# Performance work log

Hardware: AMD Instinct MI355X
Metric: run time of the kernel (lower is better)

## Reference

```python
import jax, jax.numpy as jnp
import numpy as np

REP_DIM = 256
ATT_DIM = 256
AGRU_DIM = 256
BATCH = 64
MAX_FACTS = 512


def setup_inputs() -> dict:
    key = jax.random.key(0)
    ks = jax.random.split(key, 16)

    def lin(k, out_d, in_d):
        return jax.random.normal(k, (out_d, in_d), dtype=jnp.float32) / np.sqrt(in_d)

    inp = {
        "queries": jax.random.normal(ks[0], (BATCH, 1, REP_DIM), dtype=jnp.float32),
        "facts": jax.random.normal(ks[1], (BATCH, MAX_FACTS, REP_DIM), dtype=jnp.float32),
        "num_facts": jax.random.randint(ks[2], (BATCH,), 1, MAX_FACTS + 1, dtype=jnp.int32),
        "m_old": jax.random.normal(ks[3], (BATCH, 1, REP_DIM), dtype=jnp.float32),
        # attention MLP
        "W1_w": lin(ks[4], ATT_DIM, 4 * REP_DIM),
        "W1_b": jnp.zeros((ATT_DIM,), jnp.float32),
        "W2_w": lin(ks[5], 1, ATT_DIM),
        "W2_b": jnp.zeros((1,), jnp.float32),
        # attention GRU cell
        "Wr_w": lin(ks[6], AGRU_DIM, REP_DIM),
        "Ur_w": lin(ks[7], AGRU_DIM, AGRU_DIM),
        "Ur_b": jnp.zeros((AGRU_DIM,), jnp.float32),
        "Wg_w": lin(ks[8], AGRU_DIM, REP_DIM),
        "Ug_w": lin(ks[9], AGRU_DIM, AGRU_DIM),
        "Ug_b": jnp.zeros((AGRU_DIM,), jnp.float32),
        # output transform
        "Wt_w": lin(ks[10], REP_DIM, 2 * REP_DIM + AGRU_DIM),
        "Wt_b": jnp.zeros((REP_DIM,), jnp.float32),
    }
    return inp


def _forward(queries, facts, num_facts, m_old,
             W1_w, W1_b, W2_w, W2_b,
             Wr_w, Ur_w, Ur_b, Wg_w, Ug_w, Ug_b,
             Wt_w, Wt_b):
    B, T, D = facts.shape

    # ---- attention scores ----
    q = queries  # (B,1,D) broadcasts
    m = m_old
    z = jnp.concatenate(
        [facts * q, facts * m, jnp.abs(facts - q), jnp.abs(facts - m)], axis=2
    )  # (B,T,4D)
    Z = jnp.tanh(jnp.einsum("btf,af->bta", z, W1_w) + W1_b)
    Z = jnp.einsum("bta,oa->bto", Z, W2_w) + W2_b  # (B,T,1)
    mask = (jnp.arange(T)[None, :] < num_facts[:, None])[..., None]  # (B,T,1)
    Z = jnp.where(mask, Z, -jnp.inf)
    g = jax.nn.softmax(Z, axis=1)  # (B,T,1)

    # ---- attention GRU (sequential scan over facts) ----
    h0 = m_old[:, 0]  # (B,A)

    def step(h, xs):
        fact, g_t = xs  # (B,D), (B,1)
        r = jax.nn.sigmoid(fact @ Wr_w.T + h @ Ur_w.T + Ur_b)
        h_t = jnp.tanh(fact @ Wg_w.T + r * (h @ Ug_w.T + Ug_b))
        h_new = g_t * h_t + (1.0 - g_t) * h
        return h_new, h_new

    xs = (jnp.swapaxes(facts, 0, 1), jnp.swapaxes(g, 0, 1))  # (T,B,D),(T,B,1)
    _, states = jax.lax.scan(step, h0, xs)  # (T,B,A)
    c = jnp.take_along_axis(
        states, (num_facts - 1)[None, :, None].astype(jnp.int32), axis=0
    )[0]  # (B,A)

    # ---- next memory ----
    cat = jnp.concatenate([m_old[:, 0], c, queries[:, 0]], axis=1)
    m_new = jax.nn.relu(cat @ Wt_w.T + Wt_b)
    return m_new[:, None, :]  # (B,1,D)


def reference(queries, facts, num_facts, m_old,
              W1_w, W1_b, W2_w, W2_b,
              Wr_w, Ur_w, Ur_b, Wg_w, Ug_w, Ug_b,
              Wt_w, Wt_b):
    return _forward(queries, facts, num_facts, m_old,
                    W1_w, W1_b, W2_w, W2_b,
                    Wr_w, Ur_w, Ur_b, Wg_w, Ug_w, Ug_b,
                    Wt_w, Wt_b)
```

## Files before the change

### kernel.cpp

```cpp
#include <hip/hip_runtime.h>
#include <hip/hip_fp16.h>
#include <stdint.h>

#define B 64
#define T 512
#define D 256

typedef _Float16 f16;
typedef __attribute__((ext_vector_type(8))) _Float16 f16x8;
typedef __attribute__((ext_vector_type(2))) _Float16 f16x2;
typedef __attribute__((ext_vector_type(4))) float f32x4;
typedef __attribute__((ext_vector_type(4))) unsigned int u32x4;

static __device__ __forceinline__ float dot2f(f16x2 a, f16x2 b, float c) {
  return __builtin_amdgcn_fdot2(a, b, c, false);
}
static __device__ __forceinline__ f16x2 as_h2(unsigned int u) {
  return __builtin_bit_cast(f16x2, u);
}

__global__ void k_convert(const float* __restrict__ W1, const float* __restrict__ Wr,
                          const float* __restrict__ Wg, const float* __restrict__ facts,
                          f16* __restrict__ W1h, f16* __restrict__ Wrh,
                          f16* __restrict__ Wgh, f16* __restrict__ Fh)
{
  const int64_t n1 = 256 * 1024, n2 = 65536, n3 = 65536, n4 = (int64_t)B * T * D;
  int64_t stride = (int64_t)gridDim.x * blockDim.x;
  for (int64_t i = (int64_t)blockIdx.x * blockDim.x + threadIdx.x; i < n1 + n2 + n3 + n4; i += stride) {
    if (i < n1)                W1h[i] = (f16)W1[i];
    else if (i < n1 + n2)      Wrh[i - n1] = (f16)Wr[i - n1];
    else if (i < n1 + n2 + n3) Wgh[i - n1 - n2] = (f16)Wg[i - n1 - n2];
    else                       Fh[i - n1 - n2 - n3] = (f16)facts[i - n1 - n2 - n3];
  }
}

__global__ __launch_bounds__(256, 2) void k_attn(
    const float* __restrict__ facts, const float* __restrict__ queries,
    const float* __restrict__ m_old, const f16* __restrict__ W1h,
    const float* __restrict__ W1_b, const float* __restrict__ W2_w,
    const float* __restrict__ W2_b, float* __restrict__ Zlog)
{
  const int b = blockIdx.y;
  const int t0 = blockIdx.x * 32;
  const int tid = threadIdx.x;
  const int lane = tid & 63;
  const int wave = tid >> 6;
  const int lr = lane & 15;
  const int lg = lane >> 4;

  __shared__ float q_s[D], m_s[D];
  __shared__ __align__(16) char zbuf[32 * 2048];
  __shared__ float part[4][32];

  q_s[tid] = queries[b * D + tid];
  m_s[tid] = m_old[b * D + tid];
  __syncthreads();

  for (int e = tid; e < 32 * 128; e += 256) {
    int t = e >> 7;
    int j2 = e & 127;
    int j = j2 * 2;
    const float2 f2 = *(const float2*)(facts + ((int64_t)(b * T) + t0 + t) * D + j);
    float q0 = q_s[j], q1 = q_s[j + 1], mm0 = m_s[j], mm1 = m_s[j + 1];
    f16x2 z0; z0[0] = (f16)(f2.x * q0);        z0[1] = (f16)(f2.y * q1);
    f16x2 z1; z1[0] = (f16)(f2.x * mm0);       z1[1] = (f16)(f2.y * mm1);
    f16x2 z2; z2[0] = (f16)fabsf(f2.x - q0);   z2[1] = (f16)fabsf(f2.y - q1);
    f16x2 z3; z3[0] = (f16)fabsf(f2.x - mm0);  z3[1] = (f16)fabsf(f2.y - mm1);
    int xr = (t & 7) << 4;
    int base = t * 2048;
    *(f16x2*)(zbuf + ((base + (0 * 128 + j2) * 4) ^ xr)) = z0;
    *(f16x2*)(zbuf + ((base + (1 * 128 + j2) * 4) ^ xr)) = z1;
    *(f16x2*)(zbuf + ((base + (2 * 128 + j2) * 4) ^ xr)) = z2;
    *(f16x2*)(zbuf + ((base + (3 * 128 + j2) * 4) ^ xr)) = z3;
  }
  __syncthreads();

  const int n0 = wave * 64;
  f32x4 acc[2][4];
  #pragma unroll
  for (int i = 0; i < 2; ++i)
    #pragma unroll
    for (int j = 0; j < 4; ++j) acc[i][j] = (f32x4){0.f, 0.f, 0.f, 0.f};

  #pragma unroll 2
  for (int ks = 0; ks < 32; ++ks) {
    f16x8 af[2];
    #pragma unroll
    for (int mt = 0; mt < 2; ++mt) {
      int row = mt * 16 + lr;
      int byte = (row * 2048 + ks * 64 + lg * 16) ^ ((row & 7) << 4);
      af[mt] = *(const f16x8*)(zbuf + byte);
    }
    #pragma unroll
    for (int nt = 0; nt < 4; ++nt) {
      int a = n0 + nt * 16 + lr;
      f16x8 bf = *(const f16x8*)(W1h + (int64_t)a * 1024 + ks * 32 + lg * 8);
      acc[0][nt] = __builtin_amdgcn_mfma_f32_16x16x32_f16(af[0], bf, acc[0][nt], 0, 0, 0);
      acc[1][nt] = __builtin_amdgcn_mfma_f32_16x16x32_f16(af[1], bf, acc[1][nt], 0, 0, 0);
    }
  }

  float pr[2][4] = {{0.f, 0.f, 0.f, 0.f}, {0.f, 0.f, 0.f, 0.f}};
  #pragma unroll
  for (int nt = 0; nt < 4; ++nt) {
    int a = n0 + nt * 16 + lr;
    float b1 = W1_b[a];
    float w2 = W2_w[a];
    #pragma unroll
    for (int mt = 0; mt < 2; ++mt)
      #pragma unroll
      for (int r = 0; r < 4; ++r)
        pr[mt][r] += tanhf(acc[mt][nt][r] + b1) * w2;
  }
  #pragma unroll
  for (int mt = 0; mt < 2; ++mt)
    #pragma unroll
    for (int r = 0; r < 4; ++r) {
      float v = pr[mt][r];
      v += __shfl_xor(v, 1, 64);
      v += __shfl_xor(v, 2, 64);
      v += __shfl_xor(v, 4, 64);
      v += __shfl_xor(v, 8, 64);
      pr[mt][r] = v;
    }
  if ((lane & 15) == 0) {
    #pragma unroll
    for (int mt = 0; mt < 2; ++mt)
      #pragma unroll
      for (int r = 0; r < 4; ++r)
        part[wave][mt * 16 + lg * 4 + r] = pr[mt][r];
  }
  __syncthreads();
  if (tid < 32)
    Zlog[b * T + t0 + tid] = part[0][tid] + part[1][tid] + part[2][tid] + part[3][tid] + W2_b[0];
}

__global__ __launch_bounds__(256, 2) void k_factproj(
    const f16* __restrict__ Fh, const f16* __restrict__ Wrh, const f16* __restrict__ Wgh,
    const float* __restrict__ Ur_b, float* __restrict__ Fr, float* __restrict__ Fg)
{
  const int b = blockIdx.y;
  const int t0 = blockIdx.x * 64;
  const int tid = threadIdx.x;
  const int lane = tid & 63;
  const int wave = tid >> 6;
  const int lr = lane & 15;
  const int lg = lane >> 4;

  __shared__ __align__(16) char albuf[64 * 512];

  for (int c = tid; c < 64 * 32; c += 256) {
    int row = c >> 5;
    int kc = c & 31;
    f16x8 v = *(const f16x8*)(Fh + ((int64_t)(b * T) + t0 + row) * D + kc * 8);
    int byte = (row * 512 + kc * 16) ^ ((row & 7) << 4);
    *(f16x8*)(albuf + byte) = v;
  }
  __syncthreads();

  f32x4 accr[16], accg[16];
  #pragma unroll
  for (int i = 0; i < 16; ++i) { accr[i] = (f32x4){0.f,0.f,0.f,0.f}; accg[i] = (f32x4){0.f,0.f,0.f,0.f}; }

  const int arow = wave * 16 + lr;
  #pragma unroll 2
  for (int ks = 0; ks < 8; ++ks) {
    int byte = (arow * 512 + ks * 64 + lg * 16) ^ ((arow & 7) << 4);
    f16x8 af = *(const f16x8*)(albuf + byte);
    #pragma unroll
    for (int nt = 0; nt < 16; ++nt) {
      int a = nt * 16 + lr;
      f16x8 br = *(const f16x8*)(Wrh + a * 256 + ks * 32 + lg * 8);
      f16x8 bg = *(const f16x8*)(Wgh + a * 256 + ks * 32 + lg * 8);
      accr[nt] = __builtin_amdgcn_mfma_f32_16x16x32_f16(af, br, accr[nt], 0, 0, 0);
      accg[nt] = __builtin_amdgcn_mfma_f32_16x16x32_f16(af, bg, accg[nt], 0, 0, 0);
    }
  }

  #pragma unroll
  for (int nt = 0; nt < 16; ++nt) {
    int col = nt * 16 + lr;
    float urb = Ur_b[col];
    #pragma unroll
    for (int r = 0; r < 4; ++r) {
      int t = t0 + wave * 16 + lg * 4 + r;
      int64_t off = ((int64_t)(b * T) + t) * D + col;
      Fr[off] = accr[nt][r] + urb;
      Fg[off] = accg[nt][r];
    }
  }
}

__global__ void k_softmax2(const float* __restrict__ Zlog, const int* __restrict__ num_facts,
                           float* __restrict__ g)
{
  const int b = blockIdx.x;
  const int lane = threadIdx.x;
  const int nf = num_facts[b];
  float v[8];
  float mx = -INFINITY;
  #pragma unroll
  for (int j = 0; j < 8; ++j) {
    int t = j * 64 + lane;
    float z = Zlog[b * T + t];
    v[j] = (t < nf) ? z : -INFINITY;
    mx = fmaxf(mx, v[j]);
  }
  #pragma unroll
  for (int s = 1; s < 64; s <<= 1) mx = fmaxf(mx, __shfl_xor(mx, s, 64));
  float e[8];
  float sum = 0.f;
  #pragma unroll
  for (int j = 0; j < 8; ++j) {
    int t = j * 64 + lane;
    e[j] = (t < nf) ? __expf(v[j] - mx) : 0.f;
    sum += e[j];
  }
  #pragma unroll
  for (int s = 1; s < 64; s <<= 1) sum += __shfl_xor(sum, s, 64);
  float inv = 1.f / sum;
  #pragma unroll
  for (int j = 0; j < 8; ++j)
    g[b * T + j * 64 + lane] = e[j] * inv;
}

__global__ __launch_bounds__(512, 2) void k_scan_v3(
    const float* __restrict__ Fr, const float* __restrict__ Fg, const float* __restrict__ g,
    const int* __restrict__ num_facts, const float* __restrict__ Ur_w,
    const float* __restrict__ Ug_w, const float* __restrict__ Ug_b,
    const float* __restrict__ m_old, float* __restrict__ c_out)
{
  const int b = blockIdx.x;
  const int tid = threadIdx.x;
  const int row = ((tid >> 6) << 5) + (tid & 31);
  const int kgh = (tid >> 5) & 1;
  const int nf = num_facts[b];

  __shared__ __align__(16) f16 hbuf[2][256];

  const float* __restrict__ urow = Ur_w + (int64_t)row * 256 + kgh * 128;
  const float* __restrict__ grow = Ug_w + (int64_t)row * 256 + kgh * 128;
  f16x2 wR[64], wG[64];
  #pragma unroll
  for (int j = 0; j < 64; ++j) {
    float2 a = *(const float2*)(urow + 2 * j);
    float2 c = *(const float2*)(grow + 2 * j);
    f16x2 pa; pa[0] = (f16)a.x; pa[1] = (f16)a.y; wR[j] = pa;
    f16x2 pc; pc[0] = (f16)c.x; pc[1] = (f16)c.y; wG[j] = pc;
  }
  const float ugb = Ug_b[row];
  float h = m_old[b * 256 + row];
  if (kgh == 0) hbuf[0][row] = (f16)h;
  __syncthreads();

  const float* __restrict__ FrP = Fr + (int64_t)(b * T) * D + row;
  const float* __restrict__ FgP = Fg + (int64_t)(b * T) * D + row;
  const float* __restrict__ gP  = g + b * T;
  float fr = FrP[0], fg = FgP[0], gt = gP[0];

  const f16* hc = hbuf[0];
  f16* hn = hbuf[1];

  for (int t = 0; t < nf; ++t) {
    float fr_n = 0.f, fg_n = 0.f, gt_n = 0.f;
    if (t + 1 < nf) {
      fr_n = FrP[(int64_t)(t + 1) * D];
      fg_n = FgP[(int64_t)(t + 1) * D];
      gt_n = gP[t + 1];
    }

    const u32x4* __restrict__ hp = (const u32x4*)(hc + kgh * 128);
    float r0 = 0.f, r1 = 0.f, r2 = 0.f, r3 = 0.f;
    float q0 = 0.f, q1 = 0.f, q2 = 0.f, q3 = 0.f;
    #pragma unroll
    for (int c = 0; c < 16; ++c) {
      u32x4 hv = hp[c];
      f16x2 h0 = as_h2(hv.x), h1 = as_h2(hv.y), h2 = as_h2(hv.z), h3 = as_h2(hv.w);
      r0 = dot2f(h0, wR[c * 4 + 0], r0);
      r1 = dot2f(h1, wR[c * 4 + 1], r1);
      r2 = dot2f(h2, wR[c * 4 + 2], r2);
      r3 = dot2f(h3, wR[c * 4 + 3], r3);
      q0 = dot2f(h0, wG[c * 4 + 0], q0);
      q1 = dot2f(h1, wG[c * 4 + 1], q1);
      q2 = dot2f(h2, wG[c * 4 + 2], q2);
      q3 = dot2f(h3, wG[c * 4 + 3], q3);
    }
    float dR = (r0 + r1) + (r2 + r3);
    float dG = (q0 + q1) + (q2 + q3);
    dR += __shfl_xor(dR, 32, 64);
    dG += __shfl_xor(dG, 32, 64);

    float rr = 1.f / (1.f + __expf(-(fr + dR)));
    float ht = tanhf(fg + rr * (dG + ugb));
    h = gt * ht + (1.f - gt) * h;
    if (kgh == 0) hn[row] = (f16)h;

    fr = fr_n; fg = fg_n; gt = gt_n;
    const f16* tmp = hc; hc = hn; hn = (f16*)tmp;
    __syncthreads();
  }
  if (kgh == 0) c_out[b * 256 + row] = h;
}

__global__ __launch_bounds__(256) void k_final2(
    const float* __restrict__ m_old, const float* __restrict__ c_ws,
    const float* __restrict__ queries, const float* __restrict__ Wt_w,
    const float* __restrict__ Wt_b, float* __restrict__ out)
{
  const int b = blockIdx.x;
  const int tid = threadIdx.x;
  __shared__ __align__(16) float cat_s[768];
  for (int e = tid; e < 768; e += 256) {
    float v = (e < 256) ? m_old[b * 256 + e]
            : (e < 512) ? c_ws[b * 256 + (e - 256)]
                        : queries[b * 256 + (e - 512)];
    cat_s[e] = v;
  }
  __syncthreads();
  const float* wrow = Wt_w + (int64_t)tid * 768;
  float acc = 0.f;
  #pragma unroll 8
  for (int k = 0; k < 768; k += 4) {
    float4 w = *(const float4*)(wrow + k);
    float4 c4 = *(const float4*)(cat_s + k);
    acc += w.x * c4.x + w.y * c4.y + w.z * c4.z + w.w * c4.w;
  }
  out[b * 256 + tid] = fmaxf(acc + Wt_b[tid], 0.f);
}

extern "C" void kernel_launch(void* const* d_in, const int* in_sizes, int n_in,
                              void* d_out, int out_size, void* d_ws, size_t ws_size,
                              hipStream_t stream)
{
  const float* queries   = (const float*)d_in[0];
  const float* facts     = (const float*)d_in[1];
  const int*   num_facts = (const int*)d_in[2];
  const float* m_old     = (const float*)d_in[3];
  const float* W1_w = (const float*)d_in[4];
  const float* W1_b = (const float*)d_in[5];
  const float* W2_w = (const float*)d_in[6];
  const float* W2_b = (const float*)d_in[7];
  const float* Wr_w = (const float*)d_in[8];
  const float* Ur_w = (const float*)d_in[9];
  const float* Ur_b = (const float*)d_in[10];
  const float* Wg_w = (const float*)d_in[11];
  const float* Ug_w = (const float*)d_in[12];
  const float* Ug_b = (const float*)d_in[13];
  const float* Wt_w = (const float*)d_in[14];
  const float* Wt_b = (const float*)d_in[15];
  float* out = (float*)d_out;

  char* p = (char*)d_ws;
  auto alloc = [&](size_t bytes) { char* r = p; p += (bytes + 255) & ~(size_t)255; return r; };
  f16*   W1h  = (f16*)alloc((size_t)256 * 1024 * 2);
  f16*   Wrh  = (f16*)alloc((size_t)65536 * 2);
  f16*   Wgh  = (f16*)alloc((size_t)65536 * 2);
  f16*   Fh   = (f16*)alloc((size_t)B * T * D * 2);
  float* Zlog = (float*)alloc((size_t)B * T * 4);
  float* g    = (float*)alloc((size_t)B * T * 4);
  float* Fr   = (float*)alloc((size_t)B * T * D * 4);
  float* Fg   = (float*)alloc((size_t)B * T * D * 4);
  float* c_ws = (float*)alloc((size_t)B * D * 4);

  k_convert<<<dim3(2048), dim3(256), 0, stream>>>(W1_w, Wr_w, Wg_w, facts, W1h, Wrh, Wgh, Fh);
  k_attn<<<dim3(16, 64), dim3(256), 0, stream>>>(facts, queries, m_old, W1h, W1_b, W2_w, W2_b, Zlog);
  k_factproj<<<dim3(8, 64), dim3(256), 0, stream>>>(Fh, Wrh, Wgh, Ur_b, Fr, Fg);
  k_softmax2<<<dim3(64), dim3(64), 0, stream>>>(Zlog, num_facts, g);
  k_scan_v3<<<dim3(64), dim3(512), 0, stream>>>(Fr, Fg, g, num_facts, Ur_w, Ug_w, Ug_b, m_old, c_ws);
  k_final2<<<dim3(64), dim3(256), 0, stream>>>(m_old, c_ws, queries, Wt_w, Wt_b, out);
}
```

Measured before the change: 774.0 us.

## Batch 16 sequences per scan block with MFMA and drop separate facts fp16 pass

The recurrent GRU scan now handles 16 batch rows per block. The hidden-state matvecs become 16x16x32 f16 MFMA tiles, with the recurrent weights held in registers as A fragments. It iterates to the maximum num_facts in the group and relies on zero attention weights to freeze finished sequences. The gates use rcp/exp-based sigmoid and tanh. Separately, the fp16 conversion of facts is folded into the fact-projection kernel's LDS staging, removing a full-tensor read/write pass. The trade-off is fewer scan blocks, extra steps for shorter sequences in a group, and strided per-lane Fr/Fg loads across batches.

```diff
diff --git a/kernel.cpp b/kernel.cpp
--- a/kernel.cpp
+++ b/kernel.cpp
@@ -8,29 +8,20 @@
 
 typedef _Float16 f16;
 typedef __attribute__((ext_vector_type(8))) _Float16 f16x8;
+typedef __attribute__((ext_vector_type(4))) _Float16 f16x4;
 typedef __attribute__((ext_vector_type(2))) _Float16 f16x2;
 typedef __attribute__((ext_vector_type(4))) float f32x4;
-typedef __attribute__((ext_vector_type(4))) unsigned int u32x4;
-
-static __device__ __forceinline__ float dot2f(f16x2 a, f16x2 b, float c) {
-  return __builtin_amdgcn_fdot2(a, b, c, false);
-}
-static __device__ __forceinline__ f16x2 as_h2(unsigned int u) {
-  return __builtin_bit_cast(f16x2, u);
-}
 
 __global__ void k_convert(const float* __restrict__ W1, const float* __restrict__ Wr,
-                          const float* __restrict__ Wg, const float* __restrict__ facts,
-                          f16* __restrict__ W1h, f16* __restrict__ Wrh,
-                          f16* __restrict__ Wgh, f16* __restrict__ Fh)
-{
-  const int64_t n1 = 256 * 1024, n2 = 65536, n3 = 65536, n4 = (int64_t)B * T * D;
+                          const float* __restrict__ Wg,
+                          f16* __restrict__ W1h, f16* __restrict__ Wrh, f16* __restrict__ Wgh)
+{
+  const int64_t n1 = 256 * 1024, n2 = 65536, n3 = 65536;
   int64_t stride = (int64_t)gridDim.x * blockDim.x;
-  for (int64_t i = (int64_t)blockIdx.x * blockDim.x + threadIdx.x; i < n1 + n2 + n3 + n4; i += stride) {
-    if (i < n1)                W1h[i] = (f16)W1[i];
-    else if (i < n1 + n2)      Wrh[i - n1] = (f16)Wr[i - n1];
-    else if (i < n1 + n2 + n3) Wgh[i - n1 - n2] = (f16)Wg[i - n1 - n2];
-    else                       Fh[i - n1 - n2 - n3] = (f16)facts[i - n1 - n2 - n3];
+  for (int64_t i = (int64_t)blockIdx.x * blockDim.x + threadIdx.x; i < n1 + n2 + n3; i += stride) {
+    if (i < n1)           W1h[i] = (f16)W1[i];
+    else if (i < n1 + n2) Wrh[i - n1] = (f16)Wr[i - n1];
+    else                  Wgh[i - n1 - n2] = (f16)Wg[i - n1 - n2];
   }
 }
 
@@ -136,7 +127,7 @@
 }
 
 __global__ __launch_bounds__(256, 2) void k_factproj(
-    const f16* __restrict__ Fh, const f16* __restrict__ Wrh, const f16* __restrict__ Wgh,
+    const float* __restrict__ facts, const f16* __restrict__ Wrh, const f16* __restrict__ Wgh,
     const float* __restrict__ Ur_b, float* __restrict__ Fr, float* __restrict__ Fg)
 {
   const int b = blockIdx.y;
@@ -152,7 +143,12 @@
   for (int c = tid; c < 64 * 32; c += 256) {
     int row = c >> 5;
     int kc = c & 31;
-    f16x8 v = *(const f16x8*)(Fh + ((int64_t)(b * T) + t0 + row) * D + kc * 8);
+    const float* src = facts + ((int64_t)(b * T) + t0 + row) * D + kc * 8;
+    float4 x0 = *(const float4*)src;
+    float4 x1 = *(const float4*)(src + 4);
+    f16x8 v;
+    v[0] = (f16)x0.x; v[1] = (f16)x0.y; v[2] = (f16)x0.z; v[3] = (f16)x0.w;
+    v[4] = (f16)x1.x; v[5] = (f16)x1.y; v[6] = (f16)x1.z; v[7] = (f16)x1.w;
     int byte = (row * 512 + kc * 16) ^ ((row & 7) << 4);
     *(f16x8*)(albuf + byte) = v;
   }
@@ -224,82 +220,129 @@
     g[b * T + j * 64 + lane] = e[j] * inv;
 }
 
-__global__ __launch_bounds__(512, 2) void k_scan_v3(
+__global__ __launch_bounds__(512) void k_scan_v4(
     const float* __restrict__ Fr, const float* __restrict__ Fg, const float* __restrict__ g,
     const int* __restrict__ num_facts, const float* __restrict__ Ur_w,
     const float* __restrict__ Ug_w, const float* __restrict__ Ug_b,
     const float* __restrict__ m_old, float* __restrict__ c_out)
 {
-  const int b = blockIdx.x;
+  const int b0 = blockIdx.x * 16;
   const int tid = threadIdx.x;
-  const int row = ((tid >> 6) << 5) + (tid & 31);
-  const int kgh = (tid >> 5) & 1;
-  const int nf = num_facts[b];
-
-  __shared__ __align__(16) f16 hbuf[2][256];
-
-  const float* __restrict__ urow = Ur_w + (int64_t)row * 256 + kgh * 128;
-  const float* __restrict__ grow = Ug_w + (int64_t)row * 256 + kgh * 128;
-  f16x2 wR[64], wG[64];
-  #pragma unroll
-  for (int j = 0; j < 64; ++j) {
-    float2 a = *(const float2*)(urow + 2 * j);
-    float2 c = *(const float2*)(grow + 2 * j);
-    f16x2 pa; pa[0] = (f16)a.x; pa[1] = (f16)a.y; wR[j] = pa;
-    f16x2 pc; pc[0] = (f16)c.x; pc[1] = (f16)c.y; wG[j] = pc;
-  }
-  const float ugb = Ug_b[row];
-  float h = m_old[b * 256 + row];
-  if (kgh == 0) hbuf[0][row] = (f16)h;
-  __syncthreads();
-
-  const float* __restrict__ FrP = Fr + (int64_t)(b * T) * D + row;
-  const float* __restrict__ FgP = Fg + (int64_t)(b * T) * D + row;
-  const float* __restrict__ gP  = g + b * T;
-  float fr = FrP[0], fg = FgP[0], gt = gP[0];
-
-  const f16* hc = hbuf[0];
-  f16* hn = hbuf[1];
-
-  for (int t = 0; t < nf; ++t) {
-    float fr_n = 0.f, fg_n = 0.f, gt_n = 0.f;
-    if (t + 1 < nf) {
-      fr_n = FrP[(int64_t)(t + 1) * D];
-      fg_n = FgP[(int64_t)(t + 1) * D];
-      gt_n = gP[t + 1];
-    }
-
-    const u32x4* __restrict__ hp = (const u32x4*)(hc + kgh * 128);
-    float r0 = 0.f, r1 = 0.f, r2 = 0.f, r3 = 0.f;
-    float q0 = 0.f, q1 = 0.f, q2 = 0.f, q3 = 0.f;
-    #pragma unroll
-    for (int c = 0; c < 16; ++c) {
-      u32x4 hv = hp[c];
-      f16x2 h0 = as_h2(hv.x), h1 = as_h2(hv.y), h2 = as_h2(hv.z), h3 = as_h2(hv.w);
-      r0 = dot2f(h0, wR[c * 4 + 0], r0);
-      r1 = dot2f(h1, wR[c * 4 + 1], r1);
-      r2 = dot2f(h2, wR[c * 4 + 2], r2);
-      r3 = dot2f(h3, wR[c * 4 + 3], r3);
-      q0 = dot2f(h0, wG[c * 4 + 0], q0);
-      q1 = dot2f(h1, wG[c * 4 + 1], q1);
-      q2 = dot2f(h2, wG[c * 4 + 2], q2);
-      q3 = dot2f(h3, wG[c * 4 + 3], q3);
-    }
-    float dR = (r0 + r1) + (r2 + r3);
-    float dG = (q0 + q1) + (q2 + q3);
-    dR += __shfl_xor(dR, 32, 64);
-    dG += __shfl_xor(dG, 32, 64);
-
-    float rr = 1.f / (1.f + __expf(-(fr + dR)));
-    float ht = tanhf(fg + rr * (dG + ugb));
-    h = gt * ht + (1.f - gt) * h;
-    if (kgh == 0) hn[row] = (f16)h;
-
-    fr = fr_n; fg = fg_n; gt = gt_n;
-    const f16* tmp = hc; hc = hn; hn = (f16*)tmp;
+  const int lane = tid & 63;
+  const int wave = tid >> 6;
+  const int lr = lane & 15;
+  const int lg = lane >> 4;
+
+  __shared__ __align__(16) char hbuf[2][16 * 512];
+
+  f16x8 aR[2][8], aG[2][8];
+  #pragma unroll
+  for (int rt = 0; rt < 2; ++rt) {
+    int arow = wave * 32 + rt * 16 + lr;
+    #pragma unroll
+    for (int kt = 0; kt < 8; ++kt) {
+      const float* ur = Ur_w + (int64_t)arow * 256 + kt * 32 + lg * 8;
+      const float* ug = Ug_w + (int64_t)arow * 256 + kt * 32 + lg * 8;
+      float4 u0 = *(const float4*)ur, u1 = *(const float4*)(ur + 4);
+      float4 v0 = *(const float4*)ug, v1 = *(const float4*)(ug + 4);
+      f16x8 fa, fb;
+      fa[0]=(f16)u0.x; fa[1]=(f16)u0.y; fa[2]=(f16)u0.z; fa[3]=(f16)u0.w;
+      fa[4]=(f16)u1.x; fa[5]=(f16)u1.y; fa[6]=(f16)u1.z; fa[7]=(f16)u1.w;
+      fb[0]=(f16)v0.x; fb[1]=(f16)v0.y; fb[2]=(f16)v0.z; fb[3]=(f16)v0.w;
+      fb[4]=(f16)v1.x; fb[5]=(f16)v1.y; fb[6]=(f16)v1.z; fb[7]=(f16)v1.w;
+      aR[rt][kt] = fa;
+      aG[rt][kt] = fb;
+    }
+  }
+
+  const int rbase = wave * 32 + lg * 4;
+  float4 ho[2], ugb[2];
+  #pragma unroll
+  for (int rt = 0; rt < 2; ++rt) {
+    ho[rt]  = *(const float4*)(m_old + (int64_t)(b0 + lr) * 256 + rbase + rt * 16);
+    ugb[rt] = *(const float4*)(Ug_b + rbase + rt * 16);
+  }
+
+  int nfmax = 0;
+  #pragma unroll
+  for (int j = 0; j < 16; ++j) nfmax = max(nfmax, num_facts[b0 + j]);
+
+  const int swz = (lr & 7) << 4;
+  #pragma unroll
+  for (int rt = 0; rt < 2; ++rt) {
+    f16x4 p;
+    p[0] = (f16)ho[rt].x; p[1] = (f16)ho[rt].y; p[2] = (f16)ho[rt].z; p[3] = (f16)ho[rt].w;
+    *(f16x4*)(&hbuf[0][0] + ((lr * 512 + (rbase + rt * 16) * 2) ^ swz)) = p;
+  }
+
+  const float* frp = Fr + (int64_t)(b0 + lr) * T * D + rbase;
+  const float* fgp = Fg + (int64_t)(b0 + lr) * T * D + rbase;
+  const float* gpp = g + (b0 + lr) * T;
+  float4 frv[2], fgv[2];
+  float gtv;
+  frv[0] = *(const float4*)(frp);       frv[1] = *(const float4*)(frp + 16);
+  fgv[0] = *(const float4*)(fgp);       fgv[1] = *(const float4*)(fgp + 16);
+  gtv = gpp[0];
+
+  __syncthreads();
+
+  for (int t = 0; t < nfmax; ++t) {
+    const char* hb = &hbuf[t & 1][0];
+    f16x8 bf[8];
+    #pragma unroll
+    for (int kt = 0; kt < 8; ++kt)
+      bf[kt] = *(const f16x8*)(hb + ((lr * 512 + kt * 64 + lg * 16) ^ swz));
+
+    float4 nfr0 = {0,0,0,0}, nfr1 = {0,0,0,0}, nfg0 = {0,0,0,0}, nfg1 = {0,0,0,0};
+    float ngt = 0.f;
+    if (t + 1 < nfmax) {
+      const float* fp = frp + (int64_t)(t + 1) * D;
+      const float* gp2 = fgp + (int64_t)(t + 1) * D;
+      nfr0 = *(const float4*)(fp);       nfr1 = *(const float4*)(fp + 16);
+      nfg0 = *(const float4*)(gp2);      nfg1 = *(const float4*)(gp2 + 16);
+      ngt = gpp[t + 1];
+    }
+
+    f32x4 dR[2] = {{0,0,0,0},{0,0,0,0}}, dG[2] = {{0,0,0,0},{0,0,0,0}};
+    #pragma unroll
+    for (int kt = 0; kt < 8; ++kt) {
+      dR[0] = __builtin_amdgcn_mfma_f32_16x16x32_f16(aR[0][kt], bf[kt], dR[0], 0, 0, 0);
+      dR[1] = __builtin_amdgcn_mfma_f32_16x16x32_f16(aR[1][kt], bf[kt], dR[1], 0, 0, 0);
+      dG[0] = __builtin_amdgcn_mfma_f32_16x16x32_f16(aG[0][kt], bf[kt], dG[0], 0, 0, 0);
+      dG[1] = __builtin_amdgcn_mfma_f32_16x16x32_f16(aG[1][kt], bf[kt], dG[1], 0, 0, 0);
+    }
+
+    char* hn = &hbuf[(t + 1) & 1][0];
+    #pragma unroll
+    for (int rt = 0; rt < 2; ++rt) {
+      float hr[4] = {ho[rt].x, ho[rt].y, ho[rt].z, ho[rt].w};
+      float fr4[4] = {frv[rt].x, frv[rt].y, frv[rt].z, frv[rt].w};
+      float fg4[4] = {fgv[rt].x, fgv[rt].y, fgv[rt].z, fgv[rt].w};
+      float ub4[4] = {ugb[rt].x, ugb[rt].y, ugb[rt].z, ugb[rt].w};
+      f16x4 p;
+      #pragma unroll
+      for (int r = 0; r < 4; ++r) {
+        float xr = fr4[r] + dR[rt][r];
+        float rr = __builtin_amdgcn_rcpf(1.f + __expf(-xr));
+        float y  = fg4[r] + rr * (dG[rt][r] + ub4[r]);
+        float e2 = __expf(y * 2.f);
+        float ht = 1.f - 2.f * __builtin_amdgcn_rcpf(1.f + e2);
+        float hn1 = hr[r] + gtv * (ht - hr[r]);
+        hr[r] = hn1;
+        p[r] = (f16)hn1;
+      }
+      ho[rt] = (float4){hr[0], hr[1], hr[2], hr[3]};
+      *(f16x4*)(hn + ((lr * 512 + (rbase + rt * 16) * 2) ^ swz)) = p;
+    }
+
+    frv[0] = nfr0; frv[1] = nfr1;
+    fgv[0] = nfg0; fgv[1] = nfg1;
+    gtv = ngt;
     __syncthreads();
   }
-  if (kgh == 0) c_out[b * 256 + row] = h;
+
+  *(float4*)(c_out + (int64_t)(b0 + lr) * 256 + rbase)      = ho[0];
+  *(float4*)(c_out + (int64_t)(b0 + lr) * 256 + rbase + 16) = ho[1];
 }
 
 __global__ __launch_bounds__(256) void k_final2(
@@ -355,17 +398,16 @@
   f16*   W1h  = (f16*)alloc((size_t)256 * 1024 * 2);
   f16*   Wrh  = (f16*)alloc((size_t)65536 * 2);
   f16*   Wgh  = (f16*)alloc((size_t)65536 * 2);
-  f16*   Fh   = (f16*)alloc((size_t)B * T * D * 2);
   float* Zlog = (float*)alloc((size_t)B * T * 4);
   float* g    = (float*)alloc((size_t)B * T * 4);
   float* Fr   = (float*)alloc((size_t)B * T * D * 4);
   float* Fg   = (float*)alloc((size_t)B * T * D * 4);
   float* c_ws = (float*)alloc((size_t)B * D * 4);
 
-  k_convert<<<dim3(2048), dim3(256), 0, stream>>>(W1_w, Wr_w, Wg_w, facts, W1h, Wrh, Wgh, Fh);
+  k_convert<<<dim3(768), dim3(256), 0, stream>>>(W1_w, Wr_w, Wg_w, W1h, Wrh, Wgh);
   k_attn<<<dim3(16, 64), dim3(256), 0, stream>>>(facts, queries, m_old, W1h, W1_b, W2_w, W2_b, Zlog);
-  k_factproj<<<dim3(8, 64), dim3(256), 0, stream>>>(Fh, Wrh, Wgh, Ur_b, Fr, Fg);
+  k_factproj<<<dim3(8, 64), dim3(256), 0, stream>>>(facts, Wrh, Wgh, Ur_b, Fr, Fg);
   k_softmax2<<<dim3(64), dim3(64), 0, stream>>>(Zlog, num_facts, g);
-  k_scan_v3<<<dim3(64), dim3(512), 0, stream>>>(Fr, Fg, g, num_facts, Ur_w, Ug_w, Ug_b, m_old, c_ws);
+  k_scan_v4<<<dim3(4), dim3(512), 0, stream>>>(Fr, Fg, g, num_facts, Ur_w, Ug_w, Ug_b, m_old, c_ws);
   k_final2<<<dim3(64), dim3(256), 0, stream>>>(m_old, c_ws, queries, Wt_w, Wt_b, out);
 }
```

After: 902.9 us. +16.7%, slower.

## Fuse softmax and output transform into restructured fp16 GRU scan kernel

Applied to the files above, without the earlier changes.

Removes the separate fp16 fact conversion by having the fact projection read fp32 facts directly, and stores the projected Fr/Fg in fp16 to halve their traffic. The softmax and the final linear+ReLU are folded into the scan kernel, dropping two launches and the g/c round trips. The scan is remapped so each thread owns 4 rows over a 32-wide k slice, using an 8-lane shuffle reduction and a padded LDS h buffer, with fast rcp-based sigmoid/tanh. This adds fp16 rounding of the projections and approximate transcendental error.

```diff
diff --git a/kernel.cpp b/kernel.cpp
--- a/kernel.cpp
+++ b/kernel.cpp
@@ -8,6 +8,7 @@
 
 typedef _Float16 f16;
 typedef __attribute__((ext_vector_type(8))) _Float16 f16x8;
+typedef __attribute__((ext_vector_type(4))) _Float16 f16x4;
 typedef __attribute__((ext_vector_type(2))) _Float16 f16x2;
 typedef __attribute__((ext_vector_type(4))) float f32x4;
 typedef __attribute__((ext_vector_type(4))) unsigned int u32x4;
@@ -20,17 +21,15 @@
 }
 
 __global__ void k_convert(const float* __restrict__ W1, const float* __restrict__ Wr,
-                          const float* __restrict__ Wg, const float* __restrict__ facts,
-                          f16* __restrict__ W1h, f16* __restrict__ Wrh,
-                          f16* __restrict__ Wgh, f16* __restrict__ Fh)
-{
-  const int64_t n1 = 256 * 1024, n2 = 65536, n3 = 65536, n4 = (int64_t)B * T * D;
+                          const float* __restrict__ Wg,
+                          f16* __restrict__ W1h, f16* __restrict__ Wrh, f16* __restrict__ Wgh)
+{
+  const int64_t n1 = 256 * 1024, n2 = 65536, n3 = 65536;
   int64_t stride = (int64_t)gridDim.x * blockDim.x;
-  for (int64_t i = (int64_t)blockIdx.x * blockDim.x + threadIdx.x; i < n1 + n2 + n3 + n4; i += stride) {
-    if (i < n1)                W1h[i] = (f16)W1[i];
-    else if (i < n1 + n2)      Wrh[i - n1] = (f16)Wr[i - n1];
-    else if (i < n1 + n2 + n3) Wgh[i - n1 - n2] = (f16)Wg[i - n1 - n2];
-    else                       Fh[i - n1 - n2 - n3] = (f16)facts[i - n1 - n2 - n3];
+  for (int64_t i = (int64_t)blockIdx.x * blockDim.x + threadIdx.x; i < n1 + n2 + n3; i += stride) {
+    if (i < n1)           W1h[i] = (f16)W1[i];
+    else if (i < n1 + n2) Wrh[i - n1] = (f16)Wr[i - n1];
+    else                  Wgh[i - n1 - n2] = (f16)Wg[i - n1 - n2];
   }
 }
 
@@ -136,8 +135,8 @@
 }
 
 __global__ __launch_bounds__(256, 2) void k_factproj(
-    const f16* __restrict__ Fh, const f16* __restrict__ Wrh, const f16* __restrict__ Wgh,
-    const float* __restrict__ Ur_b, float* __restrict__ Fr, float* __restrict__ Fg)
+    const float* __restrict__ facts, const f16* __restrict__ Wrh, const f16* __restrict__ Wgh,
+    const float* __restrict__ Ur_b, f16* __restrict__ Frh, f16* __restrict__ Fgh)
 {
   const int b = blockIdx.y;
   const int t0 = blockIdx.x * 64;
@@ -152,7 +151,12 @@
   for (int c = tid; c < 64 * 32; c += 256) {
     int row = c >> 5;
     int kc = c & 31;
-    f16x8 v = *(const f16x8*)(Fh + ((int64_t)(b * T) + t0 + row) * D + kc * 8);
+    const float* src = facts + ((int64_t)(b * T) + t0 + row) * D + kc * 8;
+    float4 x0 = *(const float4*)src;
+    float4 x1 = *(const float4*)(src + 4);
+    f16x8 v;
+    v[0] = (f16)x0.x; v[1] = (f16)x0.y; v[2] = (f16)x0.z; v[3] = (f16)x0.w;
+    v[4] = (f16)x1.x; v[5] = (f16)x1.y; v[6] = (f16)x1.z; v[7] = (f16)x1.w;
     int byte = (row * 512 + kc * 16) ^ ((row & 7) << 4);
     *(f16x8*)(albuf + byte) = v;
   }
@@ -185,147 +189,170 @@
     for (int r = 0; r < 4; ++r) {
       int t = t0 + wave * 16 + lg * 4 + r;
       int64_t off = ((int64_t)(b * T) + t) * D + col;
-      Fr[off] = accr[nt][r] + urb;
-      Fg[off] = accg[nt][r];
-    }
-  }
-}
-
-__global__ void k_softmax2(const float* __restrict__ Zlog, const int* __restrict__ num_facts,
-                           float* __restrict__ g)
-{
-  const int b = blockIdx.x;
-  const int lane = threadIdx.x;
-  const int nf = num_facts[b];
-  float v[8];
-  float mx = -INFINITY;
-  #pragma unroll
-  for (int j = 0; j < 8; ++j) {
-    int t = j * 64 + lane;
-    float z = Zlog[b * T + t];
-    v[j] = (t < nf) ? z : -INFINITY;
-    mx = fmaxf(mx, v[j]);
-  }
-  #pragma unroll
-  for (int s = 1; s < 64; s <<= 1) mx = fmaxf(mx, __shfl_xor(mx, s, 64));
-  float e[8];
-  float sum = 0.f;
-  #pragma unroll
-  for (int j = 0; j < 8; ++j) {
-    int t = j * 64 + lane;
-    e[j] = (t < nf) ? __expf(v[j] - mx) : 0.f;
-    sum += e[j];
-  }
-  #pragma unroll
-  for (int s = 1; s < 64; s <<= 1) sum += __shfl_xor(sum, s, 64);
-  float inv = 1.f / sum;
-  #pragma unroll
-  for (int j = 0; j < 8; ++j)
-    g[b * T + j * 64 + lane] = e[j] * inv;
-}
-
-__global__ __launch_bounds__(512, 2) void k_scan_v3(
-    const float* __restrict__ Fr, const float* __restrict__ Fg, const float* __restrict__ g,
-    const int* __restrict__ num_facts, const float* __restrict__ Ur_w,
-    const float* __restrict__ Ug_w, const float* __restrict__ Ug_b,
-    const float* __restrict__ m_old, float* __restrict__ c_out)
+      Frh[off] = (f16)(accr[nt][r] + urb);
+      Fgh[off] = (f16)(accg[nt][r]);
+    }
+  }
+}
+
+__global__ __launch_bounds__(512) void k_scan_v5(
+    const float* __restrict__ Zlog, const int* __restrict__ num_facts,
+    const f16* __restrict__ Frh, const f16* __restrict__ Fgh,
+    const float* __restrict__ Ur_w, const float* __restrict__ Ug_w,
+    const float* __restrict__ Ug_b, const float* __restrict__ m_old,
+    const float* __restrict__ queries, const float* __restrict__ Wt_w,
+    const float* __restrict__ Wt_b, float* __restrict__ out)
 {
   const int b = blockIdx.x;
   const int tid = threadIdx.x;
-  const int row = ((tid >> 6) << 5) + (tid & 31);
-  const int kgh = (tid >> 5) & 1;
+  const int l = tid & 63;
+  const int w = tid >> 6;
+  const int kg = l & 7;
+  const int rg = w * 8 + (l >> 3);
+  const int r0 = rg * 4;
   const int nf = num_facts[b];
 
-  __shared__ __align__(16) f16 hbuf[2][256];
-
-  const float* __restrict__ urow = Ur_w + (int64_t)row * 256 + kgh * 128;
-  const float* __restrict__ grow = Ug_w + (int64_t)row * 256 + kgh * 128;
-  f16x2 wR[64], wG[64];
-  #pragma unroll
-  for (int j = 0; j < 64; ++j) {
-    float2 a = *(const float2*)(urow + 2 * j);
-    float2 c = *(const float2*)(grow + 2 * j);
-    f16x2 pa; pa[0] = (f16)a.x; pa[1] = (f16)a.y; wR[j] = pa;
-    f16x2 pc; pc[0] = (f16)c.x; pc[1] = (f16)c.y; wG[j] = pc;
-  }
-  const float ugb = Ug_b[row];
-  float h = m_old[b * 256 + row];
-  if (kgh == 0) hbuf[0][row] = (f16)h;
-  __syncthreads();
-
-  const float* __restrict__ FrP = Fr + (int64_t)(b * T) * D + row;
-  const float* __restrict__ FgP = Fg + (int64_t)(b * T) * D + row;
-  const float* __restrict__ gP  = g + b * T;
-  float fr = FrP[0], fg = FgP[0], gt = gP[0];
-
-  const f16* hc = hbuf[0];
-  f16* hn = hbuf[1];
+  __shared__ __align__(16) char hbuf[2][640];
+  __shared__ float g_lds[512];
+  __shared__ float red[8];
+  __shared__ __align__(16) float cat_s[768];
+
+  {
+    float z = Zlog[b * 512 + tid];
+    float v = (tid < nf) ? z : -INFINITY;
+    float mx = v;
+    #pragma unroll
+    for (int s = 1; s < 64; s <<= 1) mx = fmaxf(mx, __shfl_xor(mx, s, 64));
+    if (l == 0) red[w] = mx;
+    __syncthreads();
+    mx = red[0];
+    #pragma unroll
+    for (int j = 1; j < 8; ++j) mx = fmaxf(mx, red[j]);
+    float e = (tid < nf) ? __expf(v - mx) : 0.f;
+    float sum = e;
+    #pragma unroll
+    for (int s = 1; s < 64; s <<= 1) sum += __shfl_xor(sum, s, 64);
+    __syncthreads();
+    if (l == 0) red[w] = sum;
+    __syncthreads();
+    sum = red[0] + red[1] + red[2] + red[3] + red[4] + red[5] + red[6] + red[7];
+    g_lds[tid] = e / sum;
+  }
+
+  f16x2 wR[4][16], wG[4][16];
+  #pragma unroll
+  for (int j = 0; j < 4; ++j) {
+    const float* ur = Ur_w + (int64_t)(r0 + j) * 256 + kg * 32;
+    const float* ug = Ug_w + (int64_t)(r0 + j) * 256 + kg * 32;
+    #pragma unroll
+    for (int q = 0; q < 8; ++q) {
+      float4 a = *(const float4*)(ur + q * 4);
+      float4 c = *(const float4*)(ug + q * 4);
+      f16x2 p0; p0[0] = (f16)a.x; p0[1] = (f16)a.y;
+      f16x2 p1; p1[0] = (f16)a.z; p1[1] = (f16)a.w;
+      f16x2 q0; q0[0] = (f16)c.x; q0[1] = (f16)c.y;
+      f16x2 q1; q1[0] = (f16)c.z; q1[1] = (f16)c.w;
+      wR[j][q * 2 + 0] = p0;
+      wR[j][q * 2 + 1] = p1;
+      wG[j][q * 2 + 0] = q0;
+      wG[j][q * 2 + 1] = q1;
+    }
+  }
+
+  float4 h0 = *(const float4*)(m_old + (int64_t)b * 256 + r0);
+  float h[4] = {h0.x, h0.y, h0.z, h0.w};
+  float4 ub4 = *(const float4*)(Ug_b + r0);
+
+  const int haddr = (r0 >> 5) * 80 + (r0 & 31) * 2;
+  if (kg == 0) {
+    f16x4 p; p[0] = (f16)h[0]; p[1] = (f16)h[1]; p[2] = (f16)h[2]; p[3] = (f16)h[3];
+    *(f16x4*)(&hbuf[0][haddr]) = p;
+  }
+
+  const f16* __restrict__ frp = Frh + (int64_t)(b * T) * D + r0;
+  const f16* __restrict__ fgp = Fgh + (int64_t)(b * T) * D + r0;
+  f16x4 frv = *(const f16x4*)frp;
+  f16x4 fgv = *(const f16x4*)fgp;
+
+  __syncthreads();
 
   for (int t = 0; t < nf; ++t) {
-    float fr_n = 0.f, fg_n = 0.f, gt_n = 0.f;
+    const char* hb = hbuf[t & 1];
+    u32x4 hv0 = *(const u32x4*)(hb + kg * 80);
+    u32x4 hv1 = *(const u32x4*)(hb + kg * 80 + 16);
+    u32x4 hv2 = *(const u32x4*)(hb + kg * 80 + 32);
+    u32x4 hv3 = *(const u32x4*)(hb + kg * 80 + 48);
+
+    f16x4 nfr = {}, nfg = {};
     if (t + 1 < nf) {
-      fr_n = FrP[(int64_t)(t + 1) * D];
-      fg_n = FgP[(int64_t)(t + 1) * D];
-      gt_n = gP[t + 1];
-    }
-
-    const u32x4* __restrict__ hp = (const u32x4*)(hc + kgh * 128);
-    float r0 = 0.f, r1 = 0.f, r2 = 0.f, r3 = 0.f;
-    float q0 = 0.f, q1 = 0.f, q2 = 0.f, q3 = 0.f;
-    #pragma unroll
-    for (int c = 0; c < 16; ++c) {
-      u32x4 hv = hp[c];
-      f16x2 h0 = as_h2(hv.x), h1 = as_h2(hv.y), h2 = as_h2(hv.z), h3 = as_h2(hv.w);
-      r0 = dot2f(h0, wR[c * 4 + 0], r0);
-      r1 = dot2f(h1, wR[c * 4 + 1], r1);
-      r2 = dot2f(h2, wR[c * 4 + 2], r2);
-      r3 = dot2f(h3, wR[c * 4 + 3], r3);
-      q0 = dot2f(h0, wG[c * 4 + 0], q0);
-      q1 = dot2f(h1, wG[c * 4 + 1], q1);
-      q2 = dot2f(h2, wG[c * 4 + 2], q2);
-      q3 = dot2f(h3, wG[c * 4 + 3], q3);
-    }
-    float dR = (r0 + r1) + (r2 + r3);
-    float dG = (q0 + q1) + (q2 + q3);
-    dR += __shfl_xor(dR, 32, 64);
-    dG += __shfl_xor(dG, 32, 64);
-
-    float rr = 1.f / (1.f + __expf(-(fr + dR)));
-    float ht = tanhf(fg + rr * (dG + ugb));
-    h = gt * ht + (1.f - gt) * h;
-    if (kgh == 0) hn[row] = (f16)h;
-
-    fr = fr_n; fg = fg_n; gt = gt_n;
-    const f16* tmp = hc; hc = hn; hn = (f16*)tmp;
+      nfr = *(const f16x4*)(frp + (int64_t)(t + 1) * D);
+      nfg = *(const f16x4*)(fgp + (int64_t)(t + 1) * D);
+    }
+    float gt = g_lds[t];
+
+    unsigned hu[16] = {hv0.x, hv0.y, hv0.z, hv0.w, hv1.x, hv1.y, hv1.z, hv1.w,
+                       hv2.x, hv2.y, hv2.z, hv2.w, hv3.x, hv3.y, hv3.z, hv3.w};
+    float aR[4] = {0.f, 0.f, 0.f, 0.f};
+    float aG[4] = {0.f, 0.f, 0.f, 0.f};
+    #pragma unroll
+    for (int i2 = 0; i2 < 16; ++i2) {
+      f16x2 hh = as_h2(hu[i2]);
+      #pragma unroll
+      for (int j = 0; j < 4; ++j) {
+        aR[j] = dot2f(hh, wR[j][i2], aR[j]);
+        aG[j] = dot2f(hh, wG[j][i2], aG[j]);
+      }
+    }
+    #pragma unroll
+    for (int s = 1; s < 8; s <<= 1) {
+      #pragma unroll
+      for (int j = 0; j < 4; ++j) {
+        aR[j] += __shfl_xor(aR[j], s, 64);
+        aG[j] += __shfl_xor(aG[j], s, 64);
+      }
+    }
+
+    f16x4 hp;
+    #pragma unroll
+    for (int j = 0; j < 4; ++j) {
+      float fr = (float)frv[j];
+      float fg = (float)fgv[j];
+      float rr = __builtin_amdgcn_rcpf(1.f + __expf(-(fr + aR[j])));
+      float y  = fg + rr * (aG[j] + ub4[j == 0 ? 0 : j]);
+      float ht = 1.f - 2.f * __builtin_amdgcn_rcpf(1.f + __expf(2.f * y));
+      h[j] = h[j] + gt * (ht - h[j]);
+      hp[j] = (f16)h[j];
+    }
+    if (kg == 0)
+      *(f16x4*)(&hbuf[(t + 1) & 1][haddr]) = hp;
+
+    frv = nfr;
+    fgv = nfg;
     __syncthreads();
   }
-  if (kgh == 0) c_out[b * 256 + row] = h;
-}
-
-__global__ __launch_bounds__(256) void k_final2(
-    const float* __restrict__ m_old, const float* __restrict__ c_ws,
-    const float* __restrict__ queries, const float* __restrict__ Wt_w,
-    const float* __restrict__ Wt_b, float* __restrict__ out)
-{
-  const int b = blockIdx.x;
-  const int tid = threadIdx.x;
-  __shared__ __align__(16) float cat_s[768];
-  for (int e = tid; e < 768; e += 256) {
-    float v = (e < 256) ? m_old[b * 256 + e]
-            : (e < 512) ? c_ws[b * 256 + (e - 256)]
-                        : queries[b * 256 + (e - 512)];
-    cat_s[e] = v;
-  }
-  __syncthreads();
-  const float* wrow = Wt_w + (int64_t)tid * 768;
-  float acc = 0.f;
-  #pragma unroll 8
-  for (int k = 0; k < 768; k += 4) {
-    float4 w = *(const float4*)(wrow + k);
-    float4 c4 = *(const float4*)(cat_s + k);
-    acc += w.x * c4.x + w.y * c4.y + w.z * c4.z + w.w * c4.w;
-  }
-  out[b * 256 + tid] = fmaxf(acc + Wt_b[tid], 0.f);
+
+  if (tid < 256) {
+    cat_s[tid]       = m_old[(int64_t)b * 256 + tid];
+    cat_s[512 + tid] = queries[(int64_t)b * 256 + tid];
+  }
+  if (kg == 0) {
+    cat_s[256 + r0 + 0] = h[0];
+    cat_s[256 + r0 + 1] = h[1];
+    cat_s[256 + r0 + 2] = h[2];
+    cat_s[256 + r0 + 3] = h[3];
+  }
+  __syncthreads();
+  if (tid < 256) {
+    const float* wrow = Wt_w + (int64_t)tid * 768;
+    float acc = 0.f;
+    #pragma unroll 8
+    for (int k = 0; k < 768; k += 4) {
+      float4 wv = *(const float4*)(wrow + k);
+      float4 c4 = *(const float4*)(cat_s + k);
+      acc += wv.x * c4.x + wv.y * c4.y + wv.z * c4.z + wv.w * c4.w;
+    }
+    out[(int64_t)b * 256 + tid] = fmaxf(acc + Wt_b[tid], 0.f);
+  }
 }
 
 extern "C" void kernel_launch(void* const* d_in, const int* in_sizes, int n_in,
@@ -355,17 +382,13 @@
   f16*   W1h  = (f16*)alloc((size_t)256 * 1024 * 2);
   f16*   Wrh  = (f16*)alloc((size_t)65536 * 2);
   f16*   Wgh  = (f16*)alloc((size_t)65536 * 2);
-  f16*   Fh   = (f16*)alloc((size_t)B * T * D * 2);
   float* Zlog = (float*)alloc((size_t)B * T * 4);
-  float* g    = (float*)alloc((size_t)B * T * 4);
-  float* Fr   = (float*)alloc((size_t)B * T * D * 4);
-  float* Fg   = (float*)alloc((size_t)B * T * D * 4);
-  float* c_ws = (float*)alloc((size_t)B * D * 4);
-
-  k_convert<<<dim3(2048), dim3(256), 0, stream>>>(W1_w, Wr_w, Wg_w, facts, W1h, Wrh, Wgh, Fh);
+  f16*   Frh  = (f16*)alloc((size_t)B * T * D * 2);
+  f16*   Fgh  = (f16*)alloc((size_t)B * T * D * 2);
+
+  k_convert<<<dim3(768), dim3(256), 0, stream>>>(W1_w, Wr_w, Wg_w, W1h, Wrh, Wgh);
   k_attn<<<dim3(16, 64), dim3(256), 0, stream>>>(facts, queries, m_old, W1h, W1_b, W2_w, W2_b, Zlog);
-  k_factproj<<<dim3(8, 64), dim3(256), 0, stream>>>(Fh, Wrh, Wgh, Ur_b, Fr, Fg);
-  k_softmax2<<<dim3(64), dim3(64), 0, stream>>>(Zlog, num_facts, g);
-  k_scan_v3<<<dim3(64), dim3(512), 0, stream>>>(Fr, Fg, g, num_facts, Ur_w, Ug_w, Ug_b, m_old, c_ws);
-  k_final2<<<dim3(64), dim3(256), 0, stream>>>(m_old, c_ws, queries, Wt_w, Wt_b, out);
-}
+  k_factproj<<<dim3(8, 64), dim3(256), 0, stream>>>(facts, Wrh, Wgh, Ur_b, Frh, Fgh);
+  k_scan_v5<<<dim3(64), dim3(512), 0, stream>>>(Zlog, num_facts, Frh, Fgh, Ur_w, Ug_w, Ug_b,
+                                                m_old, queries, Wt_w, Wt_b, out);
+}
```

After: 883.7 us. 14.2% more time.
